# Kernel optimization log

Hardware: AMD Instinct MI355X
Metric: run time of the kernel (lower is better)

## Reference

```python
import jax, jax.numpy as jnp
import numpy as np

B = 8192          # batch_size
NB = 4096         # num_banks (== mask length)
PAD = NB // 2     # reflect pad on each side


def setup_inputs() -> dict:
    key = jax.random.key(0)
    k1, k2, k3 = jax.random.split(key, 3)
    logits = jax.random.normal(k1, (NB,), dtype=jnp.float32) * 0.1
    u = jax.random.uniform(k2, (B, NB), dtype=jnp.float32)          # Bernoulli uniforms
    shift = jax.random.randint(k3, (B,), 0, NB, dtype=jnp.int32)    # per-sample shift
    return {"logits": logits, "u": u, "shift": shift}


def reference(logits, u, shift):
    # Bernoulli(sigmoid(logits)) sample via inverse-CDF on externally supplied uniforms
    p = jax.nn.sigmoid(logits)                       # (NB,)
    grid = (u < p).astype(jnp.float32)               # (B, NB)
    # Bernoulli log_prob summed over banks: g*log(p) + (1-g)*log(1-p)
    log_probs = (grid * jax.nn.log_sigmoid(logits)
                 + (1.0 - grid) * jax.nn.log_sigmoid(-logits)).sum(axis=1)  # (B,)
    # reflect-pad along bank axis, then gather a shifted window of length NB
    padded = jnp.pad(grid, ((0, 0), (PAD, PAD)), mode="reflect")    # (B, NB+2*PAD)
    idx = shift[:, None].astype(jnp.int32) + jnp.arange(NB, dtype=jnp.int32)[None, :]
    masks = jnp.take_along_axis(padded, idx, axis=1)[:, None, :]    # (B, 1, NB)
    return masks, log_probs
```

## Files before the change

kernel.cpp:

```cpp
#include <hip/hip_runtime.h>
#include <math.h>

#define NB 4096
#define PAD 2048
#define BLOCK 256
#define V4 (NB / 4 / BLOCK)

__device__ __forceinline__ int mirror_idx(int i) {
    i = ::abs(i);
    return (i < NB) ? i : (2 * (NB - 1) - i);
}

__global__ void fbmp_precompute(const float* __restrict__ logits, float* __restrict__ ws) {
    __shared__ float sred[BLOCK / 64];
    float lsnsum = 0.0f;
    for (int j = threadIdx.x; j < NB; j += BLOCK) {
        float x = logits[j];
        double xd = (double)x;
        float e = (float)exp(-xd);
        float p = 1.0f / (1.0f + e);
        float lsp = (float)(-log1p(exp(-xd)));
        float lsn = (float)(-log1p(exp(xd)));
        ws[j] = p;
        ws[NB + j] = lsp - lsn;
        lsnsum += lsn;
    }
    #pragma unroll
    for (int off = 32; off > 0; off >>= 1)
        lsnsum += __shfl_down(lsnsum, off, 64);
    const int lane = threadIdx.x & 63;
    const int wid  = threadIdx.x >> 6;
    if (lane == 0) sred[wid] = lsnsum;
    __syncthreads();
    if (threadIdx.x == 0) {
        float t = 0.0f;
        #pragma unroll
        for (int w = 0; w < BLOCK / 64; ++w) t += sred[w];
        ws[2 * NB] = t;
    }
}

__global__ __launch_bounds__(BLOCK) void fbmp_main(
    const float* __restrict__ u, const int* __restrict__ shift,
    const float* __restrict__ ws,
    float* __restrict__ masks, float* __restrict__ logp)
{
    __shared__ float sred[BLOCK / 64];

    const int b = blockIdx.x;
    const int t = threadIdx.x;
    const float* __restrict__ urow = u + (size_t)b * NB;
    const float* __restrict__ p    = ws;
    const float4* __restrict__ u4  = (const float4*)urow;
    const float4* __restrict__ p4  = (const float4*)ws;
    const float4* __restrict__ d4  = (const float4*)(ws + NB);
    const int s = shift[b] - PAD;

    float um[4 * V4];
    float pm[4 * V4];
    #pragma unroll
    for (int i = 0; i < V4; ++i) {
        #pragma unroll
        for (int e = 0; e < 4; ++e) {
            int k = 4 * (t + i * BLOCK) + e;
            int j = mirror_idx(k + s);
            um[4 * i + e] = urow[j];
            pm[4 * i + e] = p[j];
        }
    }

    float acc = 0.0f;
    #pragma unroll
    for (int i = 0; i < V4; ++i) {
        float4 uv = u4[t + i * BLOCK];
        float4 pv = p4[t + i * BLOCK];
        float4 dv = d4[t + i * BLOCK];
        acc += (uv.x < pv.x ? dv.x : 0.0f)
             + (uv.y < pv.y ? dv.y : 0.0f)
             + (uv.z < pv.z ? dv.z : 0.0f)
             + (uv.w < pv.w ? dv.w : 0.0f);
    }

    float4* __restrict__ m4 = (float4*)(masks + (size_t)b * NB);
    #pragma unroll
    for (int i = 0; i < V4; ++i) {
        float4 o;
        o.x = (um[4 * i + 0] < pm[4 * i + 0]) ? 1.0f : 0.0f;
        o.y = (um[4 * i + 1] < pm[4 * i + 1]) ? 1.0f : 0.0f;
        o.z = (um[4 * i + 2] < pm[4 * i + 2]) ? 1.0f : 0.0f;
        o.w = (um[4 * i + 3] < pm[4 * i + 3]) ? 1.0f : 0.0f;
        m4[t + i * BLOCK] = o;
    }

    #pragma unroll
    for (int off = 32; off > 0; off >>= 1)
        acc += __shfl_down(acc, off, 64);
    const int lane = t & 63;
    const int wid  = t >> 6;
    if (lane == 0) sred[wid] = acc;
    __syncthreads();
    if (t == 0) {
        float tot = 0.0f;
        #pragma unroll
        for (int w = 0; w < BLOCK / 64; ++w) tot += sred[w];
        logp[b] = tot + ws[2 * NB];
    }
}

extern "C" void kernel_launch(void* const* d_in, const int* in_sizes, int n_in,
                              void* d_out, int out_size, void* d_ws, size_t ws_size,
                              hipStream_t stream) {
    const float* logits = (const float*)d_in[0];
    const float* u      = (const float*)d_in[1];
    const int*   shift  = (const int*)d_in[2];
    const int B = in_sizes[2];

    float* ws    = (float*)d_ws;
    float* masks = (float*)d_out;
    float* logp  = (float*)d_out + (size_t)B * NB;

    fbmp_precompute<<<1, BLOCK, 0, stream>>>(logits, ws);
    fbmp_main<<<B, BLOCK, 0, stream>>>(u, shift, ws, masks, logp);
}
```

Before: 297.7 us.

## Stage Bernoulli grid row in LDS and gather shifted window from shared memory

The main kernel now reads each u row and the probability vector once with coalesced float4 loads and computes the 0/1 grid in registers. It writes that grid to a 16 KB shared-memory row, syncs, and builds the reflected, shifted mask by gathering from LDS. Before, it did scalar gathers of u and p from global memory at mirrored indices. The aim is to remove the duplicate uncoalesced global reads. The cost is 16 KB of LDS per block, which may limit occupancy, plus a block-wide barrier.

```diff
diff --git a/kernel.cpp b/kernel.cpp
--- a/kernel.cpp
+++ b/kernel.cpp
@@ -45,50 +45,51 @@
     const float* __restrict__ ws,
     float* __restrict__ masks, float* __restrict__ logp)
 {
+    __shared__ float sg[NB];
     __shared__ float sred[BLOCK / 64];
 
     const int b = blockIdx.x;
     const int t = threadIdx.x;
-    const float* __restrict__ urow = u + (size_t)b * NB;
-    const float* __restrict__ p    = ws;
-    const float4* __restrict__ u4  = (const float4*)urow;
-    const float4* __restrict__ p4  = (const float4*)ws;
-    const float4* __restrict__ d4  = (const float4*)(ws + NB);
+    const float4* __restrict__ u4 = (const float4*)(u + (size_t)b * NB);
+    const float4* __restrict__ p4 = (const float4*)ws;
+    const float4* __restrict__ d4 = (const float4*)(ws + NB);
     const int s = shift[b] - PAD;
 
-    float um[4 * V4];
-    float pm[4 * V4];
+    float4 uv[V4], pv[V4], dv[V4];
     #pragma unroll
-    for (int i = 0; i < V4; ++i) {
-        #pragma unroll
-        for (int e = 0; e < 4; ++e) {
-            int k = 4 * (t + i * BLOCK) + e;
-            int j = mirror_idx(k + s);
-            um[4 * i + e] = urow[j];
-            pm[4 * i + e] = p[j];
-        }
-    }
+    for (int i = 0; i < V4; ++i) uv[i] = u4[t + i * BLOCK];
+    #pragma unroll
+    for (int i = 0; i < V4; ++i) pv[i] = p4[t + i * BLOCK];
+    #pragma unroll
+    for (int i = 0; i < V4; ++i) dv[i] = d4[t + i * BLOCK];
 
     float acc = 0.0f;
     #pragma unroll
     for (int i = 0; i < V4; ++i) {
-        float4 uv = u4[t + i * BLOCK];
-        float4 pv = p4[t + i * BLOCK];
-        float4 dv = d4[t + i * BLOCK];
-        acc += (uv.x < pv.x ? dv.x : 0.0f)
-             + (uv.y < pv.y ? dv.y : 0.0f)
-             + (uv.z < pv.z ? dv.z : 0.0f)
-             + (uv.w < pv.w ? dv.w : 0.0f);
+        bool c0 = uv[i].x < pv[i].x;
+        bool c1 = uv[i].y < pv[i].y;
+        bool c2 = uv[i].z < pv[i].z;
+        bool c3 = uv[i].w < pv[i].w;
+        acc += (c0 ? dv[i].x : 0.0f) + (c1 ? dv[i].y : 0.0f)
+             + (c2 ? dv[i].z : 0.0f) + (c3 ? dv[i].w : 0.0f);
+        float4 g;
+        g.x = c0 ? 1.0f : 0.0f;
+        g.y = c1 ? 1.0f : 0.0f;
+        g.z = c2 ? 1.0f : 0.0f;
+        g.w = c3 ? 1.0f : 0.0f;
+        ((float4*)sg)[t + i * BLOCK] = g;
     }
+    __syncthreads();
 
     float4* __restrict__ m4 = (float4*)(masks + (size_t)b * NB);
     #pragma unroll
     for (int i = 0; i < V4; ++i) {
+        const int k = 4 * (t + i * BLOCK) + s;
         float4 o;
-        o.x = (um[4 * i + 0] < pm[4 * i + 0]) ? 1.0f : 0.0f;
-        o.y = (um[4 * i + 1] < pm[4 * i + 1]) ? 1.0f : 0.0f;
-        o.z = (um[4 * i + 2] < pm[4 * i + 2]) ? 1.0f : 0.0f;
-        o.w = (um[4 * i + 3] < pm[4 * i + 3]) ? 1.0f : 0.0f;
+        o.x = sg[mirror_idx(k + 0)];
+        o.y = sg[mirror_idx(k + 1)];
+        o.z = sg[mirror_idx(k + 2)];
+        o.w = sg[mirror_idx(k + 3)];
         m4[t + i * BLOCK] = o;
     }
 
```

Measured after the change: 247.3 us. -16.9%, faster.

## Pack Bernoulli grid into LDS bitmask and emit shifted masks from bits

Applied to the files above, without the earlier changes.

Each row's u values are now read once, coalesced. The grid bits are computed, packed into 32-bit words via cross-lane shuffles and stored in shared memory. The reflected, shifted mask window is then rebuilt from the bitmask with nibble extraction and a 4-bit reversal table, which removes the scattered scalar gathers of u and p. The change adds a raw s_waitcnt/s_barrier sequence and an occupancy hint of 8 in launch bounds. The boundary mirror logic is intricate, so correctness at the reflection edges is a risk.

```diff
diff --git a/kernel.cpp b/kernel.cpp
--- a/kernel.cpp
+++ b/kernel.cpp
@@ -1,20 +1,26 @@
 #include <hip/hip_runtime.h>
 #include <math.h>
+#include <stdint.h>
 
 #define NB 4096
 #define PAD 2048
 #define BLOCK 256
-#define V4 (NB / 4 / BLOCK)
+#define PBLOCK 256
+#define NW (NB / 32)
 
 __device__ __forceinline__ int mirror_idx(int i) {
     i = ::abs(i);
     return (i < NB) ? i : (2 * (NB - 1) - i);
 }
 
+__device__ __forceinline__ void lds_barrier() {
+    asm volatile("s_waitcnt lgkmcnt(0)\n\ts_barrier" ::: "memory");
+}
+
 __global__ void fbmp_precompute(const float* __restrict__ logits, float* __restrict__ ws) {
-    __shared__ float sred[BLOCK / 64];
+    __shared__ float sred[PBLOCK / 64];
     float lsnsum = 0.0f;
-    for (int j = threadIdx.x; j < NB; j += BLOCK) {
+    for (int j = threadIdx.x; j < NB; j += PBLOCK) {
         float x = logits[j];
         double xd = (double)x;
         float e = (float)exp(-xd);
@@ -35,74 +41,91 @@
     if (threadIdx.x == 0) {
         float t = 0.0f;
         #pragma unroll
-        for (int w = 0; w < BLOCK / 64; ++w) t += sred[w];
+        for (int w = 0; w < PBLOCK / 64; ++w) t += sred[w];
         ws[2 * NB] = t;
     }
 }
 
-__global__ __launch_bounds__(BLOCK) void fbmp_main(
+__global__ __launch_bounds__(BLOCK, 8) void fbmp_main(
     const float* __restrict__ u, const int* __restrict__ shift,
     const float* __restrict__ ws,
     float* __restrict__ masks, float* __restrict__ logp)
 {
+    __shared__ uint32_t sbits[NW + 2];
     __shared__ float sred[BLOCK / 64];
 
     const int b = blockIdx.x;
     const int t = threadIdx.x;
-    const float* __restrict__ urow = u + (size_t)b * NB;
-    const float* __restrict__ p    = ws;
-    const float4* __restrict__ u4  = (const float4*)urow;
-    const float4* __restrict__ p4  = (const float4*)ws;
-    const float4* __restrict__ d4  = (const float4*)(ws + NB);
+    const int lane = t & 63;
+    const int w = t >> 6;
+
+    const float4* __restrict__ u4 = (const float4*)(u + (size_t)b * NB);
+    const float4* __restrict__ p4 = (const float4*)ws;
+    const float4* __restrict__ d4 = (const float4*)(ws + NB);
     const int s = shift[b] - PAD;
-
-    float um[4 * V4];
-    float pm[4 * V4];
-    #pragma unroll
-    for (int i = 0; i < V4; ++i) {
-        #pragma unroll
-        for (int e = 0; e < 4; ++e) {
-            int k = 4 * (t + i * BLOCK) + e;
-            int j = mirror_idx(k + s);
-            um[4 * i + e] = urow[j];
-            pm[4 * i + e] = p[j];
-        }
-    }
 
     float acc = 0.0f;
     #pragma unroll
-    for (int i = 0; i < V4; ++i) {
-        float4 uv = u4[t + i * BLOCK];
-        float4 pv = p4[t + i * BLOCK];
-        float4 dv = d4[t + i * BLOCK];
-        acc += (uv.x < pv.x ? dv.x : 0.0f)
-             + (uv.y < pv.y ? dv.y : 0.0f)
-             + (uv.z < pv.z ? dv.z : 0.0f)
-             + (uv.w < pv.w ? dv.w : 0.0f);
-    }
-
-    float4* __restrict__ m4 = (float4*)(masks + (size_t)b * NB);
-    #pragma unroll
-    for (int i = 0; i < V4; ++i) {
-        float4 o;
-        o.x = (um[4 * i + 0] < pm[4 * i + 0]) ? 1.0f : 0.0f;
-        o.y = (um[4 * i + 1] < pm[4 * i + 1]) ? 1.0f : 0.0f;
-        o.z = (um[4 * i + 2] < pm[4 * i + 2]) ? 1.0f : 0.0f;
-        o.w = (um[4 * i + 3] < pm[4 * i + 3]) ? 1.0f : 0.0f;
-        m4[t + i * BLOCK] = o;
+    for (int i = 0; i < 4; ++i) {
+        const int f = i * BLOCK + t;
+        float4 uv = u4[f];
+        float4 pv = p4[f];
+        float4 dv = d4[f];
+        bool c0 = uv.x < pv.x;
+        bool c1 = uv.y < pv.y;
+        bool c2 = uv.z < pv.z;
+        bool c3 = uv.w < pv.w;
+        acc += (c0 ? dv.x : 0.0f) + (c1 ? dv.y : 0.0f)
+             + (c2 ? dv.z : 0.0f) + (c3 ? dv.w : 0.0f);
+        uint32_t n = (c0 ? 1u : 0u) | (c1 ? 2u : 0u) | (c2 ? 4u : 0u) | (c3 ? 8u : 0u);
+        uint32_t v = n | (((uint32_t)__shfl_xor((int)n, 1, 64)) << 4);
+        v |= ((uint32_t)__shfl_xor((int)v, 2, 64)) << 8;
+        v |= ((uint32_t)__shfl_xor((int)v, 4, 64)) << 16;
+        if ((t & 7) == 0) sbits[i * (BLOCK / 8) + (t >> 3)] = v;
     }
 
     #pragma unroll
     for (int off = 32; off > 0; off >>= 1)
         acc += __shfl_down(acc, off, 64);
-    const int lane = t & 63;
-    const int wid  = t >> 6;
-    if (lane == 0) sred[wid] = acc;
-    __syncthreads();
+    if (lane == 0) sred[w] = acc;
+
+    lds_barrier();
+
+    const uint64_t REV4 = 0xF7B3D591E6A2C480ull;
+    float4* __restrict__ m4 = (float4*)(masks + (size_t)b * NB);
+    #pragma unroll
+    for (int i = 0; i < 4; ++i) {
+        const int q = 4 * w + i;
+        const int f = 256 * q + 4 * lane + s;
+        float4 o;
+        if (f >= -3 && f <= 4095 && (f < 0 || f > 4092)) {
+            float* po = &o.x;
+            #pragma unroll
+            for (int e = 0; e < 4; ++e) {
+                int j = mirror_idx(f + e);
+                po[e] = (float)((sbits[j >> 5] >> (j & 31)) & 1u);
+            }
+        } else {
+            int sb; bool rev;
+            if (f >= 0 && f <= 4092)      { sb = f;        rev = false; }
+            else if (f < 0)               { sb = -f - 3;   rev = true;  }
+            else                          { sb = 8187 - f; rev = true;  }
+            uint32_t w0 = sbits[sb >> 5];
+            uint32_t w1 = sbits[(sb >> 5) + 1];
+            uint32_t nib = (uint32_t)((((uint64_t)w1 << 32) | w0) >> (sb & 31)) & 0xFu;
+            if (rev) nib = (uint32_t)(REV4 >> (nib << 2)) & 0xFu;
+            o.x = (nib & 1u) ? 1.0f : 0.0f;
+            o.y = (nib & 2u) ? 1.0f : 0.0f;
+            o.z = (nib & 4u) ? 1.0f : 0.0f;
+            o.w = (nib & 8u) ? 1.0f : 0.0f;
+        }
+        m4[q * 64 + lane] = o;
+    }
+
     if (t == 0) {
         float tot = 0.0f;
         #pragma unroll
-        for (int w = 0; w < BLOCK / 64; ++w) tot += sred[w];
+        for (int ww = 0; ww < BLOCK / 64; ++ww) tot += sred[ww];
         logp[b] = tot + ws[2 * NB];
     }
 }
@@ -119,6 +142,6 @@
     float* masks = (float*)d_out;
     float* logp  = (float*)d_out + (size_t)B * NB;
 
-    fbmp_precompute<<<1, BLOCK, 0, stream>>>(logits, ws);
+    fbmp_precompute<<<1, PBLOCK, 0, stream>>>(logits, ws);
     fbmp_main<<<B, BLOCK, 0, stream>>>(u, shift, ws, masks, logp);
 }
```

Result: faster. 253.9 us (-14.7%).
